# Kernel optimization log

Hardware: AMD Instinct MI355X
Metric: run time of the kernel (lower is better)

The kernel has to match this reference:

```python
import jax, jax.numpy as jnp
import numpy as np

SMALL = 1e-16
N = 8192      # num_nodes
D_IN = 512    # input_dim
D_LAT = 128   # latent_dim


def setup_inputs() -> dict:
    key = jax.random.key(0)
    ks = jax.random.split(key, 6)
    z = jax.random.normal(ks[0], (N, D_IN), jnp.float32)
    gamma = jax.random.uniform(ks[1], (N, D_IN), jnp.float32)
    delta = jax.random.uniform(ks[2], (N, D_IN), jnp.float32)
    lim = float(np.sqrt(6.0 / (D_IN + D_LAT)))  # glorot-uniform init
    Wz = jax.random.uniform(ks[3], (D_IN, D_LAT), jnp.float32, -lim, lim)
    Wg = jax.random.uniform(ks[4], (D_IN, D_LAT), jnp.float32, -lim, lim)
    Wd = jax.random.uniform(ks[5], (D_IN, D_LAT), jnp.float32, -lim, lim)
    return {
        "z": z, "gamma": gamma, "delta": delta,
        "Wz": Wz, "Wg": Wg, "Wd": Wd,
        "bias": jnp.float32(1.0),
        "w_gam": jnp.float32(0.5),
        "w_del": jnp.float32(0.5),
    }


def reference(z, gamma, delta, Wz, Wg, Wd, bias, w_gam, w_del):
    # column-stochastic transforms (softmax over input_dim axis, as in __init__)
    Tz = jax.nn.softmax(Wz, axis=0)
    Tg = jax.nn.softmax(Wg, axis=0)
    Td = jax.nn.softmax(Wd, axis=0)

    zd = z @ Tz                 # [N, D_LAT]
    gd_raw = gamma @ Tg         # [N, D_LAT]
    dd_raw = delta @ Td         # [N, D_LAT]
    gd = gd_raw + SMALL
    dd = dd_raw + SMALL

    z2 = zd * zd
    # dist_gam[i,j] = sum_k (zd[i,k]-zd[j,k])^2 / gd[i,k]  (sender-scaled)
    # expanded: sum_k z2_i/g_i  +  (1/g_i) . z2_j  -  2 (z_i/g_i) . z_j
    a = jnp.sum(z2 / gd, axis=1)                                  # [N]
    dist_gam = a[:, None] + (1.0 / gd) @ z2.T - 2.0 * (zd / gd) @ zd.T  # [N,N]

    # dist_del[i,j] = sum_k (zd[i,k]-zd[j,k])^2 / dd[j,k]  (receiver-scaled)
    b = jnp.sum(z2 / dd, axis=1)                                  # [N]
    dist_del = z2 @ (1.0 / dd).T - 2.0 * zd @ (zd / dd).T + b[None, :]  # [N,N]

    n = jnp.float32(N)
    x = bias - w_gam * (n * dist_gam) - w_del * (n * dist_del)
    out = jax.nn.sigmoid(x.reshape(-1))                           # [N*N]
    return out, zd, gd_raw, dd_raw
```

## Files before the change

### kernel.cpp

```cpp
#include <hip/hip_runtime.h>
#include <hip/hip_bf16.h>
#include <math.h>


#define NSZ 8192
#define DLAT 128

typedef _Float16 half8 __attribute__((ext_vector_type(8)));
typedef float f32x4 __attribute__((ext_vector_type(4)));

__global__ void softmax_cols(const float* __restrict__ Wz, const float* __restrict__ Wg,
                             const float* __restrict__ Wd, float* __restrict__ T) {
    int col = blockIdx.x & 127;
    int m = blockIdx.x >> 7;
    const float* W = (m == 0) ? Wz : (m == 1 ? Wg : Wd);
    float* To = T + (size_t)m * 65536;
    int l = threadIdx.x;
    float v[8];
    float mx = -3.4e38f;
    for (int i = 0; i < 8; ++i) {
        v[i] = W[(size_t)(i * 64 + l) * 128 + col];
        mx = fmaxf(mx, v[i]);
    }
    for (int off = 32; off; off >>= 1) mx = fmaxf(mx, __shfl_xor(mx, off));
    float s = 0.f;
    for (int i = 0; i < 8; ++i) { v[i] = expf(v[i] - mx); s += v[i]; }
    for (int off = 32; off; off >>= 1) s += __shfl_xor(s, off);
    float inv = 1.0f / s;
    for (int i = 0; i < 8; ++i) To[(size_t)(i * 64 + l) * 128 + col] = v[i] * inv;
}

__global__ __launch_bounds__(256) void gemm3(const float* __restrict__ z,
                                             const float* __restrict__ gamma,
                                             const float* __restrict__ delta,
                                             const float* __restrict__ T,
                                             float* __restrict__ outTail) {
    int m = blockIdx.y;
    const float* A = (m == 0) ? z : (m == 1 ? gamma : delta);
    const float* B = T + (size_t)m * 65536;
    float* C = outTail + (size_t)m * (NSZ * DLAT);
    int rowBase = blockIdx.x * 64;
    __shared__ float As[32][68];
    __shared__ float Bs[32][132];
    int t = threadIdx.x;
    int cg = t & 15, rg = t >> 4;
    float acc[4][8] = {};
    for (int kt = 0; kt < 16; ++kt) {
        int k0 = kt * 32;
        for (int i = 0; i < 2; ++i) {
            int lin = i * 1024 + t * 4;
            int r = lin >> 5, kk = lin & 31;
            float4 va = *(const float4*)(A + (size_t)(rowBase + r) * 512 + k0 + kk);
            As[kk + 0][r] = va.x; As[kk + 1][r] = va.y;
            As[kk + 2][r] = va.z; As[kk + 3][r] = va.w;
        }
        for (int i = 0; i < 4; ++i) {
            int lin = i * 1024 + t * 4;
            int kk = lin >> 7, col = lin & 127;
            *(float4*)(&Bs[kk][col]) = *(const float4*)(B + (size_t)(k0 + kk) * 128 + col);
        }
        __syncthreads();
        for (int kk = 0; kk < 32; ++kk) {
            float a0[4], b0[8];
            *(float4*)a0 = *(const float4*)(&As[kk][rg * 4]);
            *(float4*)b0 = *(const float4*)(&Bs[kk][cg * 8]);
            *(float4*)(b0 + 4) = *(const float4*)(&Bs[kk][cg * 8 + 4]);
            for (int r = 0; r < 4; ++r)
                for (int c = 0; c < 8; ++c) acc[r][c] = fmaf(a0[r], b0[c], acc[r][c]);
        }
        __syncthreads();
    }
    for (int r = 0; r < 4; ++r) {
        int row = rowBase + rg * 4 + r;
        float4 s0 = make_float4(acc[r][0], acc[r][1], acc[r][2], acc[r][3]);
        float4 s1 = make_float4(acc[r][4], acc[r][5], acc[r][6], acc[r][7]);
        *(float4*)(C + (size_t)row * 128 + cg * 8) = s0;
        *(float4*)(C + (size_t)row * 128 + cg * 8 + 4) = s1;
    }
}

__global__ void build_stacks(const float* __restrict__ zd, const float* __restrict__ gdr,
                             const float* __restrict__ ddr, _Float16* __restrict__ Afp,
                             _Float16* __restrict__ Bfp, float* __restrict__ cvec,
                             float* __restrict__ bco, const float* __restrict__ pb,
                             const float* __restrict__ pwg, const float* __restrict__ pwd) {
    int i = blockIdx.x;
    int k = threadIdx.x;
    float zv = zd[(size_t)i * 128 + k];
    float g = gdr[(size_t)i * 128 + k] + 1e-16f;
    float d = ddr[(size_t)i * 128 + k] + 1e-16f;
    float z2 = zv * zv;
    float u = 1.0f / g, p = 1.0f / d;
    float v = zv * u, q = zv * p;
    float wg = *pwg, wd = *pwd, bias = *pb;
    _Float16* Ar = Afp + (size_t)i * 512;
    _Float16* Br = Bfp + (size_t)i * 512;
    Ar[k]       = (_Float16)(wg * u);
    Ar[128 + k] = (_Float16)(wg * v);
    Ar[256 + k] = (_Float16)(wd * z2);
    Ar[384 + k] = (_Float16)(wd * zv);
    Br[k]       = (_Float16)(z2);
    Br[128 + k] = (_Float16)(-2.0f * zv);
    Br[256 + k] = (_Float16)(p);
    Br[384 + k] = (_Float16)(-2.0f * q);
    float a = z2 * u, b = z2 * p;
    for (int off = 32; off; off >>= 1) { a += __shfl_down(a, off); b += __shfl_down(b, off); }
    __shared__ float sa[2], sb[2];
    if ((k & 63) == 0) { sa[k >> 6] = a; sb[k >> 6] = b; }
    __syncthreads();
    if (k == 0) {
        cvec[i] = bias - 8192.0f * wg * (sa[0] + sa[1]);
        bco[i] = 8192.0f * wd * (sb[0] + sb[1]);
    }
}

__global__ __launch_bounds__(256) void pair_kernel(const _Float16* __restrict__ Afp,
                                                   const _Float16* __restrict__ Bfp,
                                                   const float* __restrict__ cvec,
                                                   const float* __restrict__ bco,
                                                   const float* __restrict__ pbias,
                                                   float* __restrict__ out) {
    int bid = blockIdx.x;
    int super = bid >> 6, within = bid & 63;
    int sy = super >> 3, sx = super & 7;
    int by = sy * 8 + (within >> 3), bx = sx * 8 + (within & 7);
    int iBase = by * 128, jBase = bx * 128;

    __shared__ _Float16 As[128 * 72];
    __shared__ _Float16 Bs[128 * 72];
    int t = threadIdx.x;
    int l = t & 63, w = t >> 6;
    int wm = (w >> 1) * 64, wn = (w & 1) * 64;
    int lc = l & 15, lq = l >> 4;
    f32x4 acc[4][4] = {};

    for (int kt = 0; kt < 8; ++kt) {
        int k0 = kt * 64;
        for (int i = 0; i < 4; ++i) {
            int id = i * 256 + t;
            int row = id >> 3, pos = id & 7;
            *(uint4*)(&As[row * 72 + pos * 8]) =
                *(const uint4*)(Afp + (size_t)(iBase + row) * 512 + k0 + pos * 8);
            *(uint4*)(&Bs[row * 72 + pos * 8]) =
                *(const uint4*)(Bfp + (size_t)(jBase + row) * 512 + k0 + pos * 8);
        }
        __syncthreads();
        for (int ks = 0; ks < 2; ++ks) {
            half8 af[4], bf[4];
            for (int mi = 0; mi < 4; ++mi)
                af[mi] = *(const half8*)(&As[(wm + mi * 16 + lc) * 72 + ks * 32 + lq * 8]);
            for (int ni = 0; ni < 4; ++ni)
                bf[ni] = *(const half8*)(&Bs[(wn + ni * 16 + lc) * 72 + ks * 32 + lq * 8]);
            for (int mi = 0; mi < 4; ++mi)
                for (int ni = 0; ni < 4; ++ni)
                    acc[mi][ni] = __builtin_amdgcn_mfma_f32_16x16x32_f16(af[mi], bf[ni],
                                                                         acc[mi][ni], 0, 0, 0);
        }
        __syncthreads();
    }

    float bias = *pbias;
    float civ[4][4], bjv[4];
    for (int mi = 0; mi < 4; ++mi)
        for (int r = 0; r < 4; ++r)
            civ[mi][r] = cvec[iBase + wm + mi * 16 + lq * 4 + r];
    for (int ni = 0; ni < 4; ++ni) bjv[ni] = bco[jBase + wn + ni * 16 + lc];

    for (int mi = 0; mi < 4; ++mi) {
        for (int ni = 0; ni < 4; ++ni) {
            for (int r = 0; r < 4; ++r) {
                int i = iBase + wm + mi * 16 + lq * 4 + r;
                int j = jBase + wn + ni * 16 + lc;
                float x = civ[mi][r] - bjv[ni] - 8192.0f * acc[mi][ni][r];
                if (i == j) x = bias;
                out[(size_t)i * NSZ + j] = 1.0f / (1.0f + expf(-x));
            }
        }
    }
}

extern "C" void kernel_launch(void* const* d_in, const int* in_sizes, int n_in,
                              void* d_out, int out_size, void* d_ws, size_t ws_size,
                              hipStream_t stream) {
    const float* z = (const float*)d_in[0];
    const float* gamma = (const float*)d_in[1];
    const float* delta = (const float*)d_in[2];
    const float* Wz = (const float*)d_in[3];
    const float* Wg = (const float*)d_in[4];
    const float* Wd = (const float*)d_in[5];
    const float* pb = (const float*)d_in[6];
    const float* pwg = (const float*)d_in[7];
    const float* pwd = (const float*)d_in[8];

    float* out = (float*)d_out;
    float* zd_out = out + (size_t)NSZ * NSZ;
    float* gd_out = zd_out + (size_t)NSZ * DLAT;
    float* dd_out = gd_out + (size_t)NSZ * DLAT;

    float* wsf = (float*)d_ws;
    float* T = wsf;
    float* cvec = wsf + 196608;
    float* bco = cvec + 8192;
    _Float16* Afp = (_Float16*)(bco + 8192);
    _Float16* Bfp = Afp + (size_t)NSZ * 512;

    softmax_cols<<<384, 64, 0, stream>>>(Wz, Wg, Wd, T);
    gemm3<<<dim3(128, 3), 256, 0, stream>>>(z, gamma, delta, T, zd_out);
    build_stacks<<<NSZ, 128, 0, stream>>>(zd_out, gd_out, dd_out, Afp, Bfp, cvec, bco,
                                          pb, pwg, pwd);
    pair_kernel<<<4096, 256, 0, stream>>>(Afp, Bfp, cvec, bco, pb, out);
}
```

Before: 472.6 us.

## Use direct global-to-LDS loads with XOR swizzle in pair kernel; shrink gemm3 tiles

The pair kernel now stages A/B fp16 tiles through global_load_lds (bypassing registers) into an unpadded LDS layout with an XOR swizzle on 16-byte chunks to avoid bank conflicts, and reads fragments with the matching swizzle. Separately, the fp32 projection GEMM uses 32-row tiles instead of 64, doubling the grid to 768 blocks for better CU occupancy. The pair kernel is dominated by the 256MB fp32 output write, so the load-path change may matter little; the swizzle must stay consistent or results break.

```diff
diff --git a/kernel.cpp b/kernel.cpp
--- a/kernel.cpp
+++ b/kernel.cpp
@@ -8,6 +8,12 @@
 
 typedef _Float16 half8 __attribute__((ext_vector_type(8)));
 typedef float f32x4 __attribute__((ext_vector_type(4)));
+
+__device__ __forceinline__ void gl_lds16(const void* g, void* l) {
+    __builtin_amdgcn_global_load_lds(
+        (const __attribute__((address_space(1))) void*)g,
+        (__attribute__((address_space(3))) void*)l, 16, 0, 0);
+}
 
 __global__ void softmax_cols(const float* __restrict__ Wz, const float* __restrict__ Wg,
                              const float* __restrict__ Wd, float* __restrict__ T) {
@@ -39,39 +45,40 @@
     const float* A = (m == 0) ? z : (m == 1 ? gamma : delta);
     const float* B = T + (size_t)m * 65536;
     float* C = outTail + (size_t)m * (NSZ * DLAT);
-    int rowBase = blockIdx.x * 64;
-    __shared__ float As[32][68];
-    __shared__ float Bs[32][132];
+    int rowBase = blockIdx.x * 32;
+    __shared__ float As[32 * 38];
+    __shared__ float Bs[32 * 132];
     int t = threadIdx.x;
     int cg = t & 15, rg = t >> 4;
-    float acc[4][8] = {};
+    float acc[2][8] = {};
     for (int kt = 0; kt < 16; ++kt) {
         int k0 = kt * 32;
-        for (int i = 0; i < 2; ++i) {
-            int lin = i * 1024 + t * 4;
-            int r = lin >> 5, kk = lin & 31;
+        {
+            int r = t >> 3, kk = (t & 7) * 4;
             float4 va = *(const float4*)(A + (size_t)(rowBase + r) * 512 + k0 + kk);
-            As[kk + 0][r] = va.x; As[kk + 1][r] = va.y;
-            As[kk + 2][r] = va.z; As[kk + 3][r] = va.w;
+            As[(kk + 0) * 38 + r] = va.x; As[(kk + 1) * 38 + r] = va.y;
+            As[(kk + 2) * 38 + r] = va.z; As[(kk + 3) * 38 + r] = va.w;
         }
         for (int i = 0; i < 4; ++i) {
             int lin = i * 1024 + t * 4;
             int kk = lin >> 7, col = lin & 127;
-            *(float4*)(&Bs[kk][col]) = *(const float4*)(B + (size_t)(k0 + kk) * 128 + col);
+            *(float4*)(&Bs[kk * 132 + col]) = *(const float4*)(B + (size_t)(k0 + kk) * 128 + col);
         }
         __syncthreads();
         for (int kk = 0; kk < 32; ++kk) {
-            float a0[4], b0[8];
-            *(float4*)a0 = *(const float4*)(&As[kk][rg * 4]);
-            *(float4*)b0 = *(const float4*)(&Bs[kk][cg * 8]);
-            *(float4*)(b0 + 4) = *(const float4*)(&Bs[kk][cg * 8 + 4]);
-            for (int r = 0; r < 4; ++r)
-                for (int c = 0; c < 8; ++c) acc[r][c] = fmaf(a0[r], b0[c], acc[r][c]);
-        }
-        __syncthreads();
-    }
-    for (int r = 0; r < 4; ++r) {
-        int row = rowBase + rg * 4 + r;
+            float2 av = *(const float2*)(&As[kk * 38 + rg * 2]);
+            float b0[8];
+            *(float4*)b0 = *(const float4*)(&Bs[kk * 132 + cg * 8]);
+            *(float4*)(b0 + 4) = *(const float4*)(&Bs[kk * 132 + cg * 8 + 4]);
+            for (int c = 0; c < 8; ++c) {
+                acc[0][c] = fmaf(av.x, b0[c], acc[0][c]);
+                acc[1][c] = fmaf(av.y, b0[c], acc[1][c]);
+            }
+        }
+        __syncthreads();
+    }
+    for (int r = 0; r < 2; ++r) {
+        int row = rowBase + rg * 2 + r;
         float4 s0 = make_float4(acc[r][0], acc[r][1], acc[r][2], acc[r][3]);
         float4 s1 = make_float4(acc[r][4], acc[r][5], acc[r][6], acc[r][7]);
         *(float4*)(C + (size_t)row * 128 + cg * 8) = s0;
@@ -126,31 +133,41 @@
     int by = sy * 8 + (within >> 3), bx = sx * 8 + (within & 7);
     int iBase = by * 128, jBase = bx * 128;
 
-    __shared__ _Float16 As[128 * 72];
-    __shared__ _Float16 Bs[128 * 72];
+    __shared__ _Float16 As[128 * 64];
+    __shared__ _Float16 Bs[128 * 64];
     int t = threadIdx.x;
     int l = t & 63, w = t >> 6;
     int wm = (w >> 1) * 64, wn = (w & 1) * 64;
     int lc = l & 15, lq = l >> 4;
     f32x4 acc[4][4] = {};
 
+    int srow = l >> 3;
+    int sq = (l & 7) ^ srow;
+    f32x4* accp = &acc[0][0];
+    (void)accp;
+
     for (int kt = 0; kt < 8; ++kt) {
         int k0 = kt * 64;
-        for (int i = 0; i < 4; ++i) {
-            int id = i * 256 + t;
-            int row = id >> 3, pos = id & 7;
-            *(uint4*)(&As[row * 72 + pos * 8]) =
-                *(const uint4*)(Afp + (size_t)(iBase + row) * 512 + k0 + pos * 8);
-            *(uint4*)(&Bs[row * 72 + pos * 8]) =
-                *(const uint4*)(Bfp + (size_t)(jBase + row) * 512 + k0 + pos * 8);
+        for (int s = 0; s < 4; ++s) {
+            int rr = (w * 4 + s) * 8 + srow;
+            const _Float16* ga = Afp + (size_t)(iBase + rr) * 512 + k0 + sq * 8;
+            const _Float16* gb = Bfp + (size_t)(jBase + rr) * 512 + k0 + sq * 8;
+            gl_lds16(ga, &As[(w * 4 + s) * 512]);
+            gl_lds16(gb, &Bs[(w * 4 + s) * 512]);
         }
         __syncthreads();
         for (int ks = 0; ks < 2; ++ks) {
             half8 af[4], bf[4];
-            for (int mi = 0; mi < 4; ++mi)
-                af[mi] = *(const half8*)(&As[(wm + mi * 16 + lc) * 72 + ks * 32 + lq * 8]);
-            for (int ni = 0; ni < 4; ++ni)
-                bf[ni] = *(const half8*)(&Bs[(wn + ni * 16 + lc) * 72 + ks * 32 + lq * 8]);
+            for (int mi = 0; mi < 4; ++mi) {
+                int r = wm + mi * 16 + lc;
+                int q = ks * 4 + lq;
+                af[mi] = *(const half8*)(&As[((r << 3) + (q ^ (r & 7))) << 3]);
+            }
+            for (int ni = 0; ni < 4; ++ni) {
+                int r = wn + ni * 16 + lc;
+                int q = ks * 4 + lq;
+                bf[ni] = *(const half8*)(&Bs[((r << 3) + (q ^ (r & 7))) << 3]);
+            }
             for (int mi = 0; mi < 4; ++mi)
                 for (int ni = 0; ni < 4; ++ni)
                     acc[mi][ni] = __builtin_amdgcn_mfma_f32_16x16x32_f16(af[mi], bf[ni],
@@ -205,7 +222,7 @@
     _Float16* Bfp = Afp + (size_t)NSZ * 512;
 
     softmax_cols<<<384, 64, 0, stream>>>(Wz, Wg, Wd, T);
-    gemm3<<<dim3(128, 3), 256, 0, stream>>>(z, gamma, delta, T, zd_out);
+    gemm3<<<dim3(256, 3), 256, 0, stream>>>(z, gamma, delta, T, zd_out);
     build_stacks<<<NSZ, 128, 0, stream>>>(zd_out, gd_out, dd_out, Afp, Bfp, cvec, bco,
                                           pb, pwg, pwd);
     pair_kernel<<<4096, 256, 0, stream>>>(Afp, Bfp, cvec, bco, pb, out);
```

Measured after the change: 478.8 us. No clear change (+1.3%).
